# Kernel optimization log

Measured on AMD Instinct MI355X. Metric: run time of the kernel, lower is better.

The kernel has to match this reference:

```python
import jax, jax.numpy as jnp
import numpy as np

B, S, H, D = 4, 1024, 16, 64
DM = H * D  # 1024
SCALE = float(np.sqrt(D))


def setup_inputs() -> dict:
    key = jax.random.key(0)
    ks = jax.random.split(key, 7)
    mk = lambda k, shp: jax.random.normal(k, shp, dtype=jnp.float32)
    return {
        "query": mk(ks[0], (B, S, DM)),
        "key": mk(ks[1], (B, S, DM)),
        "value": mk(ks[2], (B, S, DM)),
        "Wq": mk(ks[3], (DM, DM)) * 0.02,
        "Wk": mk(ks[4], (DM, DM)) * 0.02,
        "Wv": mk(ks[5], (DM, DM)) * 0.02,
        "Wo": mk(ks[6], (DM, DM)) * 0.02,
    }


def reference(query, key, value, Wq, Wk, Wv, Wo):
    b, s, _ = query.shape
    # nn.Linear(x) = x @ W.T ; reshape to (b, h, s, d)
    Q = (query @ Wq.T).reshape(b, s, H, D).transpose(0, 2, 1, 3)
    K = (key @ Wk.T).reshape(b, s, H, D).transpose(0, 2, 1, 3)
    V = (value @ Wv.T).reshape(b, s, H, D).transpose(0, 2, 1, 3)
    scores = jnp.einsum("bhqd,bhkd->bhqk", Q, K) / SCALE
    attn = jax.nn.softmax(scores, axis=-1)  # dropout p=0 -> identity
    ctx = jnp.einsum("bhqk,bhkd->bhqd", attn, V)
    ctx = ctx.transpose(0, 2, 1, 3).reshape(b, s, DM)
    out = ctx @ Wo.T
    return out, attn
```

## Files before the change

### kernel.cpp

```cpp
#include <hip/hip_runtime.h>
#include <hip/hip_bf16.h>
#include <stdint.h>


#define DEV static __device__ __forceinline__

typedef __bf16 bf16x8 __attribute__((ext_vector_type(8)));
typedef float f32x4 __attribute__((ext_vector_type(4)));
typedef unsigned short u16x8 __attribute__((ext_vector_type(8)));

static constexpr int B = 4, S = 1024, H = 16, D = 64, DM = 1024, M = 4096;
static constexpr size_t NQ = (size_t)M * DM;

DEV uint16_t f2bf_bits(float f) {
    __hip_bfloat16 h = __float2bfloat16(f);
    return __builtin_bit_cast(uint16_t, h);
}
DEV uint64_t pack4(float4 v) {
    return (uint64_t)f2bf_bits(v.x) | ((uint64_t)f2bf_bits(v.y) << 16) |
           ((uint64_t)f2bf_bits(v.z) << 32) | ((uint64_t)f2bf_bits(v.w) << 48);
}
DEV uint64_t pack4f(const f32x4& v) {
    return (uint64_t)f2bf_bits(v[0]) | ((uint64_t)f2bf_bits(v[1]) << 16) |
           ((uint64_t)f2bf_bits(v[2]) << 32) | ((uint64_t)f2bf_bits(v[3]) << 48);
}
DEV bf16x8 ldfrag(const uint16_t* p) {
    u16x8 t = *(const u16x8*)p;
    return __builtin_bit_cast(bf16x8, t);
}

#define GLOAD16(g, l)                                                  \
    __builtin_amdgcn_global_load_lds(                                  \
        (const __attribute__((address_space(1))) void*)(g),            \
        (__attribute__((address_space(3))) void*)(l), 16, 0, 0)

#define MFMA16(a, b, c) __builtin_amdgcn_mfma_f32_16x16x32_bf16(a, b, c, 0, 0, 0)

__global__ __launch_bounds__(256) void cvt_all(const float* __restrict__ q,
                                               const float* __restrict__ k,
                                               const float* __restrict__ v,
                                               const float* __restrict__ wq,
                                               const float* __restrict__ wk,
                                               const float* __restrict__ wv,
                                               const float* __restrict__ wo,
                                               uint16_t* __restrict__ dst) {
    const int y = blockIdx.y;
    const float* srcs[7] = {q, k, v, wq, wk, wv, wo};
    const float* src = srcs[y];
    const size_t base = y < 3 ? (size_t)y * NQ : 3 * NQ + (size_t)(y - 3) * (DM * DM);
    const size_t n = y < 3 ? NQ : (size_t)DM * DM;
    size_t i = ((size_t)blockIdx.x * 256 + threadIdx.x) * 8;
    if (i >= n) return;
    float4 a = *(const float4*)(src + i);
    float4 b2 = *(const float4*)(src + i + 4);
    *(uint64_t*)(dst + base + i) = pack4(a);
    *(uint64_t*)(dst + base + i + 4) = pack4(b2);
}

__global__ __launch_bounds__(256) void cvt_w4(const float* __restrict__ w0,
                                              const float* __restrict__ w1,
                                              const float* __restrict__ w2,
                                              const float* __restrict__ w3,
                                              uint16_t* __restrict__ dst) {
    const float* srcs[4] = {w0, w1, w2, w3};
    const float* src = srcs[blockIdx.y];
    uint16_t* d = dst + (size_t)blockIdx.y * DM * DM;
    int i = (blockIdx.x * 256 + threadIdx.x) * 8;
    float4 a = *(const float4*)(src + i);
    float4 b2 = *(const float4*)(src + i + 4);
    *(uint64_t*)(d + i) = pack4(a);
    *(uint64_t*)(d + i + 4) = pack4(b2);
}

template <int AF32>
__global__ __launch_bounds__(256) void gemm_qkv(const float* __restrict__ qa,
                                                const float* __restrict__ ka,
                                                const float* __restrict__ va,
                                                const uint16_t* __restrict__ xb,
                                                const uint16_t* __restrict__ Wb,
                                                uint16_t* __restrict__ Qb,
                                                uint16_t* __restrict__ Kb,
                                                uint16_t* __restrict__ Vt) {
    constexpr int BK = 64, ALD = AF32 ? 72 : 64;
    __shared__ __align__(16) uint16_t smem[17408];
    uint16_t* Ah = smem;
    uint16_t* Bh = smem + (AF32 ? 9216 : 8192);
    const int tid = threadIdx.x, lane = tid & 63, wid = tid >> 6;
    const int lr = lane & 15, lg = lane >> 4;
    const int m0 = blockIdx.x * 128, n0 = blockIdx.y * 128, z = blockIdx.z;
    const int wr = (wid >> 1) * 64, wc = (wid & 1) * 64;

    const float* Af = z == 0 ? qa : (z == 1 ? ka : va);
    const uint16_t* Ab = xb + (size_t)z * NQ;
    const uint16_t* W = Wb + (size_t)z * (DM * DM);

    f32x4 acc[4][4] = {};

    for (int kb = 0; kb < DM / BK; ++kb) {
        if constexpr (AF32) {
#pragma unroll
            for (int i = 0; i < 8; ++i) {
                int f = tid + i * 256;
                int row = f >> 4, c4 = (f & 15) * 4;
                float4 vv = *(const float4*)(Af + (size_t)(m0 + row) * DM + kb * BK + c4);
                *(uint64_t*)&Ah[row * ALD + c4] = pack4(vv);
            }
        } else {
#pragma unroll
            for (int p = 0; p < 4; ++p) {
                int row = p * 32 + (tid >> 3), ce = (tid & 7) * 8;
                GLOAD16(Ab + (size_t)(m0 + row) * DM + kb * BK + ce, Ah + row * 64 + ce);
            }
        }
#pragma unroll
        for (int p = 0; p < 4; ++p) {
            int row = p * 32 + (tid >> 3), ce = (tid & 7) * 8;
            GLOAD16(W + (size_t)(n0 + row) * DM + kb * BK + ce, Bh + row * 64 + ce);
        }
        __syncthreads();

        bf16x8 af[4][2], bw[4][2];
#pragma unroll
        for (int i = 0; i < 4; ++i)
#pragma unroll
            for (int ks = 0; ks < 2; ++ks) {
                af[i][ks] = ldfrag(&Ah[(wr + i * 16 + lr) * ALD + ks * 32 + lg * 8]);
                bw[i][ks] = ldfrag(&Bh[(wc + i * 16 + lr) * 64 + ks * 32 + lg * 8]);
            }
#pragma unroll
        for (int ks = 0; ks < 2; ++ks)
#pragma unroll
            for (int mi = 0; mi < 4; ++mi)
#pragma unroll
                for (int ni = 0; ni < 4; ++ni)
                    acc[mi][ni] = MFMA16(af[mi][ks], bw[ni][ks], acc[mi][ni]);
        __syncthreads();
    }

    if (z != 2) {
        uint16_t* Cp = z == 0 ? Qb : Kb;
#pragma unroll
        for (int mi = 0; mi < 4; ++mi)
#pragma unroll
            for (int ni = 0; ni < 4; ++ni)
#pragma unroll
                for (int r = 0; r < 4; ++r) {
                    int gm = m0 + wr + mi * 16 + lg * 4 + r;
                    int gn = n0 + wc + ni * 16 + lr;
                    int b = gm >> 10, s = gm & 1023, h = gn >> 6, d = gn & 63;
                    Cp[((size_t)(b * H + h) * S + s) * D + d] = f2bf_bits(acc[mi][ni][r]);
                }
    } else {
        uint16_t* T = smem;
#pragma unroll
        for (int mi = 0; mi < 4; ++mi)
#pragma unroll
            for (int ni = 0; ni < 4; ++ni) {
                int row = wc + ni * 16 + lr;
                int colb = wr + mi * 16 + lg * 4;
                *(uint64_t*)&T[row * 136 + colb] = pack4f(acc[mi][ni]);
            }
        __syncthreads();
        const int b = m0 >> 10, s0b = m0 & 1023;
#pragma unroll
        for (int p = 0; p < 8; ++p) {
            int row = p * 16 + (tid >> 4), sl = tid & 15;
            int h = (n0 + row) >> 6, d = (n0 + row) & 63;
            u16x8 val = *(u16x8*)&T[row * 136 + sl * 8];
            *(u16x8*)&Vt[((size_t)(b * H + h) * D + d) * S + s0b + sl * 8] = val;
        }
    }
}

__global__ __launch_bounds__(256) void gemm_o(const uint16_t* __restrict__ ctx,
                                              const uint16_t* __restrict__ Wo,
                                              float* __restrict__ out) {
    constexpr int BK = 64;
    __shared__ __align__(16) uint16_t smem[16384];
    uint16_t* Ah = smem;
    uint16_t* Bh = smem + 8192;
    const int tid = threadIdx.x, lane = tid & 63, wid = tid >> 6;
    const int lr = lane & 15, lg = lane >> 4;
    const int m0 = blockIdx.x * 128, n0 = blockIdx.y * 128;
    const int wr = (wid >> 1) * 64, wc = (wid & 1) * 64;

    f32x4 acc[4][4] = {};

    for (int kb = 0; kb < DM / BK; ++kb) {
#pragma unroll
        for (int p = 0; p < 4; ++p) {
            int row = p * 32 + (tid >> 3), ce = (tid & 7) * 8;
            GLOAD16(ctx + (size_t)(m0 + row) * DM + kb * BK + ce, Ah + row * 64 + ce);
            GLOAD16(Wo + (size_t)(n0 + row) * DM + kb * BK + ce, Bh + row * 64 + ce);
        }
        __syncthreads();

        bf16x8 af[4][2], bw[4][2];
#pragma unroll
        for (int i = 0; i < 4; ++i)
#pragma unroll
            for (int ks = 0; ks < 2; ++ks) {
                af[i][ks] = ldfrag(&Ah[(wr + i * 16 + lr) * 64 + ks * 32 + lg * 8]);
                bw[i][ks] = ldfrag(&Bh[(wc + i * 16 + lr) * 64 + ks * 32 + lg * 8]);
            }
#pragma unroll
        for (int ks = 0; ks < 2; ++ks)
#pragma unroll
            for (int mi = 0; mi < 4; ++mi)
#pragma unroll
                for (int ni = 0; ni < 4; ++ni)
                    acc[mi][ni] = MFMA16(af[mi][ks], bw[ni][ks], acc[mi][ni]);
        __syncthreads();
    }

#pragma unroll
    for (int mi = 0; mi < 4; ++mi)
#pragma unroll
        for (int ni = 0; ni < 4; ++ni)
#pragma unroll
            for (int r = 0; r < 4; ++r) {
                int gm = m0 + wr + mi * 16 + lg * 4 + r;
                int gn = n0 + wc + ni * 16 + lr;
                out[(size_t)gm * DM + gn] = acc[mi][ni][r];
            }
}

__global__ __launch_bounds__(256) void attn_fused(const uint16_t* __restrict__ Qb,
                                                  const uint16_t* __restrict__ Kb,
                                                  const uint16_t* __restrict__ Vt,
                                                  float* __restrict__ attn,
                                                  uint16_t* __restrict__ ctx) {
    __shared__ __align__(16) uint16_t Kl[2][2048];
    __shared__ __align__(16) uint16_t Vl[2][2048];
    __shared__ __align__(16) float pf[4][16 * 36];
    const int tid = threadIdx.x, lane = tid & 63, wid = tid >> 6;
    const int lr = lane & 15, lg = lane >> 4;
    const int wg = blockIdx.x;
    const int xcd = wg & 7, rr_ = wg >> 3;
    const int qt = rr_ & 15, bh = xcd + 8 * (rr_ >> 4);
    const int q0 = qt * 64 + wid * 16;

    const uint16_t* Qp = Qb + ((size_t)bh * S + q0) * D;
    const bf16x8 aq0 = ldfrag(Qp + lr * D + lg * 8);
    const bf16x8 aq1 = ldfrag(Qp + lr * D + 32 + lg * 8);

    const uint16_t* Kbase = Kb + (size_t)bh * S * D;
    const uint16_t* Vbase = Vt + (size_t)bh * D * S;
    constexpr float CEXP = 0.125f * 1.44269504088896340736f;

    const int krow = tid >> 3, kslot = (tid & 7) ^ ((tid >> 3) & 7);
    const int vrow = tid >> 2, vslot = (tid & 3) ^ ((tid >> 3) & 3);

#define STAGE_K(buf, kc) GLOAD16(Kbase + (size_t)((kc)*32 + krow) * D + kslot * 8, &Kl[buf][tid * 8])
#define STAGE_V(buf, kc) GLOAD16(Vbase + (size_t)vrow * S + (kc)*32 + vslot * 8, &Vl[buf][tid * 8])
#define KFRAG(buf, t, h) ldfrag(&Kl[buf][((t)*16 + lr) * 64 + ((((h)*4 + lg) ^ (lr & 7)) * 8)])
#define VFRAG(buf, dt) ldfrag(&Vl[buf][((dt)*16 + lr) * 32 + ((lg ^ ((lr >> 1) & 3)) * 8)])

    float lsum[4] = {0.f, 0.f, 0.f, 0.f};
    STAGE_K(0, 0);
    __syncthreads();
    for (int kc = 0; kc < S / 32; ++kc) {
        const int buf = kc & 1;
        if (kc < S / 32 - 1) STAGE_K(buf ^ 1, kc + 1);
        bf16x8 k00 = KFRAG(buf, 0, 0), k01 = KFRAG(buf, 0, 1);
        bf16x8 k10 = KFRAG(buf, 1, 0), k11 = KFRAG(buf, 1, 1);
        f32x4 s0 = {}, s1 = {};
        s0 = MFMA16(aq0, k00, s0);
        s0 = MFMA16(aq1, k01, s0);
        s1 = MFMA16(aq0, k10, s1);
        s1 = MFMA16(aq1, k11, s1);
#pragma unroll
        for (int r = 0; r < 4; ++r)
            lsum[r] += exp2f(s0[r] * CEXP) + exp2f(s1[r] * CEXP);
        __syncthreads();
    }
#pragma unroll
    for (int r = 0; r < 4; ++r) {
        float v = lsum[r];
        v += __shfl_xor(v, 1);
        v += __shfl_xor(v, 2);
        v += __shfl_xor(v, 4);
        v += __shfl_xor(v, 8);
        lsum[r] = 1.0f / v;
    }

    f32x4 cacc[4] = {};
    float* attn_base = attn + (size_t)bh * S * S + (size_t)q0 * S;
    float* pfw = pf[wid];

    STAGE_K(0, 0);
    STAGE_V(0, 0);
    __syncthreads();
    for (int kc = 0; kc < S / 32; ++kc) {
        const int buf = kc & 1;
        if (kc < S / 32 - 1) {
            STAGE_K(buf ^ 1, kc + 1);
            STAGE_V(buf ^ 1, kc + 1);
        }
        bf16x8 k00 = KFRAG(buf, 0, 0), k01 = KFRAG(buf, 0, 1);
        bf16x8 k10 = KFRAG(buf, 1, 0), k11 = KFRAG(buf, 1, 1);
        f32x4 s0 = {}, s1 = {};
        s0 = MFMA16(aq0, k00, s0);
        s0 = MFMA16(aq1, k01, s0);
        s1 = MFMA16(aq0, k10, s1);
        s1 = MFMA16(aq1, k11, s1);
#pragma unroll
        for (int r = 0; r < 4; ++r) {
            pfw[(lg * 4 + r) * 36 + lr] = exp2f(s0[r] * CEXP) * lsum[r];
            pfw[(lg * 4 + r) * 36 + 16 + lr] = exp2f(s1[r] * CEXP) * lsum[r];
        }
        asm volatile("s_waitcnt lgkmcnt(0)" ::: "memory");
        {
            const float* rp = &pfw[(lane >> 2) * 36 + (lane & 3) * 4];
            float4 a0 = *(const float4*)rp;
            float4 a1 = *(const float4*)(rp + 16);
            float* gp = attn_base + (size_t)(lane >> 2) * S + kc * 32 + (lane & 3) * 4;
            *(float4*)gp = a0;
            *(float4*)(gp + 16) = a1;
        }
        bf16x8 pa;
        {
            const f32x4 p0 = *(const f32x4*)&pfw[lr * 36 + lg * 8];
            const f32x4 p1 = *(const f32x4*)&pfw[lr * 36 + lg * 8 + 4];
            u16x8 pu;
#pragma unroll
            for (int j = 0; j < 4; ++j) {
                pu[j] = f2bf_bits(p0[j]);
                pu[4 + j] = f2bf_bits(p1[j]);
            }
            pa = __builtin_bit_cast(bf16x8, pu);
        }
#pragma unroll
        for (int dt = 0; dt < 4; ++dt) {
            bf16x8 bv = VFRAG(buf, dt);
            cacc[dt] = MFMA16(pa, bv, cacc[dt]);
        }
        __syncthreads();
    }

    const int b = bh >> 4, h = bh & 15;
#pragma unroll
    for (int dt = 0; dt < 4; ++dt)
#pragma unroll
        for (int r = 0; r < 4; ++r) {
            int q = q0 + lg * 4 + r;
            int d = dt * 16 + lr;
            ctx[((size_t)b * S + q) * DM + h * D + d] = f2bf_bits(cacc[dt][r]);
        }
#undef STAGE_K
#undef STAGE_V
#undef KFRAG
#undef VFRAG
}

extern "C" void kernel_launch(void* const* d_in, const int* in_sizes, int n_in,
                              void* d_out, int out_size, void* d_ws, size_t ws_size,
                              hipStream_t stream) {
    const float* q = (const float*)d_in[0];
    const float* k = (const float*)d_in[1];
    const float* v = (const float*)d_in[2];
    const float* Wq = (const float*)d_in[3];
    const float* Wk = (const float*)d_in[4];
    const float* Wv = (const float*)d_in[5];
    const float* Wo = (const float*)d_in[6];

    float* out = (float*)d_out;
    float* attn = out + (size_t)B * S * DM;

    const bool big = ws_size >= (size_t)7 * NQ * 2 + 256;
    dim3 gg(M / 128, DM / 128, 3);

    if (big) {
        uint16_t* xb = (uint16_t*)d_ws;
        uint16_t* Wb = xb + 3 * NQ;
        uint16_t* Qb = Wb + NQ;
        uint16_t* Kb = Qb + NQ;
        uint16_t* Vt = Kb + NQ;
        uint16_t* ctx = xb;
        cvt_all<<<dim3(2048, 7), 256, 0, stream>>>(q, k, v, Wq, Wk, Wv, Wo, xb);
        gemm_qkv<0><<<gg, 256, 0, stream>>>(q, k, v, xb, Wb, Qb, Kb, Vt);
        attn_fused<<<dim3(1024), 256, 0, stream>>>(Qb, Kb, Vt, attn, ctx);
        gemm_o<<<dim3(M / 128, DM / 128), 256, 0, stream>>>(ctx, Wb + (size_t)3 * DM * DM, out);
    } else {
        uint16_t* Qb = (uint16_t*)d_ws;
        uint16_t* Kb = Qb + NQ;
        uint16_t* Vt = Kb + NQ;
        uint16_t* ctx = Vt + NQ;
        uint16_t* Wb = ctx + NQ;
        cvt_w4<<<dim3(512, 4), 256, 0, stream>>>(Wq, Wk, Wv, Wo, Wb);
        gemm_qkv<1><<<gg, 256, 0, stream>>>(q, k, v, nullptr, Wb, Qb, Kb, Vt);
        attn_fused<<<dim3(1024), 256, 0, stream>>>(Qb, Kb, Vt, attn, ctx);
        gemm_o<<<dim3(M / 128, DM / 128), 256, 0, stream>>>(ctx, Wb + (size_t)3 * DM * DM, out);
    }
}
```

Baseline: 456.9 us.

## Split attention key range across warps, drop LDS staging, halve gemm_o N tile

The attention kernel now gives each block 32 queries and has two warps per query group each cover half the key range. The partial softmax denominators and context accumulators are combined through shared memory. K and V fragments are read straight from global memory instead of through double-buffered LDS with per-iteration barriers, and the attn tensor is written with nontemporal stores. This doubles the grid and raises occupancy, at the cost of uncoalesced global fragment loads and a cross-warp reduction. gemm_o switches to 128x64 tiles so it launches more blocks.

```diff
diff --git a/kernel.cpp b/kernel.cpp
--- a/kernel.cpp
+++ b/kernel.cpp
@@ -176,39 +176,46 @@
                                               const uint16_t* __restrict__ Wo,
                                               float* __restrict__ out) {
     constexpr int BK = 64;
-    __shared__ __align__(16) uint16_t smem[16384];
+    __shared__ __align__(16) uint16_t smem[(128 + 64) * BK];
     uint16_t* Ah = smem;
-    uint16_t* Bh = smem + 8192;
+    uint16_t* Bh = smem + 128 * 64;
     const int tid = threadIdx.x, lane = tid & 63, wid = tid >> 6;
     const int lr = lane & 15, lg = lane >> 4;
-    const int m0 = blockIdx.x * 128, n0 = blockIdx.y * 128;
-    const int wr = (wid >> 1) * 64, wc = (wid & 1) * 64;
-
-    f32x4 acc[4][4] = {};
+    const int m0 = blockIdx.x * 128, n0 = blockIdx.y * 64;
+    const int wr = (wid >> 1) * 64, wc = (wid & 1) * 32;
+
+    f32x4 acc[4][2] = {};
 
     for (int kb = 0; kb < DM / BK; ++kb) {
 #pragma unroll
         for (int p = 0; p < 4; ++p) {
             int row = p * 32 + (tid >> 3), ce = (tid & 7) * 8;
             GLOAD16(ctx + (size_t)(m0 + row) * DM + kb * BK + ce, Ah + row * 64 + ce);
+        }
+#pragma unroll
+        for (int p = 0; p < 2; ++p) {
+            int row = p * 32 + (tid >> 3), ce = (tid & 7) * 8;
             GLOAD16(Wo + (size_t)(n0 + row) * DM + kb * BK + ce, Bh + row * 64 + ce);
         }
         __syncthreads();
 
-        bf16x8 af[4][2], bw[4][2];
+        bf16x8 af[4][2], bw[2][2];
 #pragma unroll
         for (int i = 0; i < 4; ++i)
 #pragma unroll
-            for (int ks = 0; ks < 2; ++ks) {
+            for (int ks = 0; ks < 2; ++ks)
                 af[i][ks] = ldfrag(&Ah[(wr + i * 16 + lr) * 64 + ks * 32 + lg * 8]);
+#pragma unroll
+        for (int i = 0; i < 2; ++i)
+#pragma unroll
+            for (int ks = 0; ks < 2; ++ks)
                 bw[i][ks] = ldfrag(&Bh[(wc + i * 16 + lr) * 64 + ks * 32 + lg * 8]);
-            }
 #pragma unroll
         for (int ks = 0; ks < 2; ++ks)
 #pragma unroll
             for (int mi = 0; mi < 4; ++mi)
 #pragma unroll
-                for (int ni = 0; ni < 4; ++ni)
+                for (int ni = 0; ni < 2; ++ni)
                     acc[mi][ni] = MFMA16(af[mi][ks], bw[ni][ks], acc[mi][ni]);
         __syncthreads();
     }
@@ -216,7 +223,7 @@
 #pragma unroll
     for (int mi = 0; mi < 4; ++mi)
 #pragma unroll
-        for (int ni = 0; ni < 4; ++ni)
+        for (int ni = 0; ni < 2; ++ni)
 #pragma unroll
             for (int r = 0; r < 4; ++r) {
                 int gm = m0 + wr + mi * 16 + lg * 4 + r;
@@ -225,45 +232,38 @@
             }
 }
 
-__global__ __launch_bounds__(256) void attn_fused(const uint16_t* __restrict__ Qb,
-                                                  const uint16_t* __restrict__ Kb,
-                                                  const uint16_t* __restrict__ Vt,
-                                                  float* __restrict__ attn,
-                                                  uint16_t* __restrict__ ctx) {
-    __shared__ __align__(16) uint16_t Kl[2][2048];
-    __shared__ __align__(16) uint16_t Vl[2][2048];
+__global__ __launch_bounds__(256, 8) void attn_fused(const uint16_t* __restrict__ Qb,
+                                                     const uint16_t* __restrict__ Kb,
+                                                     const uint16_t* __restrict__ Vt,
+                                                     float* __restrict__ attn,
+                                                     uint16_t* __restrict__ ctx) {
     __shared__ __align__(16) float pf[4][16 * 36];
+    __shared__ __align__(16) float redc[2][16 * 68];
+    __shared__ float redl[2][2][16];
     const int tid = threadIdx.x, lane = tid & 63, wid = tid >> 6;
     const int lr = lane & 15, lg = lane >> 4;
+    const int qg = wid >> 1, kh = wid & 1;
     const int wg = blockIdx.x;
-    const int xcd = wg & 7, rr_ = wg >> 3;
-    const int qt = rr_ & 15, bh = xcd + 8 * (rr_ >> 4);
-    const int q0 = qt * 64 + wid * 16;
+    const int xcd = wg & 7, rr = wg >> 3;
+    const int qt = rr & 31, bh = xcd + 8 * (rr >> 5);
+    const int q0 = qt * 32 + qg * 16;
+    const int kb0 = kh * 512;
 
     const uint16_t* Qp = Qb + ((size_t)bh * S + q0) * D;
     const bf16x8 aq0 = ldfrag(Qp + lr * D + lg * 8);
     const bf16x8 aq1 = ldfrag(Qp + lr * D + 32 + lg * 8);
 
-    const uint16_t* Kbase = Kb + (size_t)bh * S * D;
-    const uint16_t* Vbase = Vt + (size_t)bh * D * S;
+    const uint16_t* Kbase = Kb + ((size_t)bh * S + kb0) * D;
+    const uint16_t* Vbase = Vt + (size_t)bh * D * S + kb0;
     constexpr float CEXP = 0.125f * 1.44269504088896340736f;
 
-    const int krow = tid >> 3, kslot = (tid & 7) ^ ((tid >> 3) & 7);
-    const int vrow = tid >> 2, vslot = (tid & 3) ^ ((tid >> 3) & 3);
-
-#define STAGE_K(buf, kc) GLOAD16(Kbase + (size_t)((kc)*32 + krow) * D + kslot * 8, &Kl[buf][tid * 8])
-#define STAGE_V(buf, kc) GLOAD16(Vbase + (size_t)vrow * S + (kc)*32 + vslot * 8, &Vl[buf][tid * 8])
-#define KFRAG(buf, t, h) ldfrag(&Kl[buf][((t)*16 + lr) * 64 + ((((h)*4 + lg) ^ (lr & 7)) * 8)])
-#define VFRAG(buf, dt) ldfrag(&Vl[buf][((dt)*16 + lr) * 32 + ((lg ^ ((lr >> 1) & 3)) * 8)])
-
     float lsum[4] = {0.f, 0.f, 0.f, 0.f};
-    STAGE_K(0, 0);
-    __syncthreads();
-    for (int kc = 0; kc < S / 32; ++kc) {
-        const int buf = kc & 1;
-        if (kc < S / 32 - 1) STAGE_K(buf ^ 1, kc + 1);
-        bf16x8 k00 = KFRAG(buf, 0, 0), k01 = KFRAG(buf, 0, 1);
-        bf16x8 k10 = KFRAG(buf, 1, 0), k11 = KFRAG(buf, 1, 1);
+    for (int kc = 0; kc < 16; ++kc) {
+        const uint16_t* Kp = Kbase + (size_t)kc * 32 * D;
+        bf16x8 k00 = ldfrag(Kp + lr * D + lg * 8);
+        bf16x8 k01 = ldfrag(Kp + lr * D + 32 + lg * 8);
+        bf16x8 k10 = ldfrag(Kp + (16 + lr) * D + lg * 8);
+        bf16x8 k11 = ldfrag(Kp + (16 + lr) * D + 32 + lg * 8);
         f32x4 s0 = {}, s1 = {};
         s0 = MFMA16(aq0, k00, s0);
         s0 = MFMA16(aq1, k01, s0);
@@ -272,7 +272,6 @@
 #pragma unroll
         for (int r = 0; r < 4; ++r)
             lsum[r] += exp2f(s0[r] * CEXP) + exp2f(s1[r] * CEXP);
-        __syncthreads();
     }
 #pragma unroll
     for (int r = 0; r < 4; ++r) {
@@ -281,24 +280,31 @@
         v += __shfl_xor(v, 2);
         v += __shfl_xor(v, 4);
         v += __shfl_xor(v, 8);
-        lsum[r] = 1.0f / v;
-    }
+        lsum[r] = v;
+    }
+    if (lr == 0) {
+#pragma unroll
+        for (int r = 0; r < 4; ++r) redl[qg][kh][lg * 4 + r] = lsum[r];
+    }
+    __syncthreads();
+    float linv[4];
+#pragma unroll
+    for (int r = 0; r < 4; ++r) linv[r] = 1.0f / (lsum[r] + redl[qg][kh ^ 1][lg * 4 + r]);
 
     f32x4 cacc[4] = {};
-    float* attn_base = attn + (size_t)bh * S * S + (size_t)q0 * S;
+    float* attn_base = attn + (size_t)bh * S * S + (size_t)q0 * S + kb0;
     float* pfw = pf[wid];
 
-    STAGE_K(0, 0);
-    STAGE_V(0, 0);
-    __syncthreads();
-    for (int kc = 0; kc < S / 32; ++kc) {
-        const int buf = kc & 1;
-        if (kc < S / 32 - 1) {
-            STAGE_K(buf ^ 1, kc + 1);
-            STAGE_V(buf ^ 1, kc + 1);
-        }
-        bf16x8 k00 = KFRAG(buf, 0, 0), k01 = KFRAG(buf, 0, 1);
-        bf16x8 k10 = KFRAG(buf, 1, 0), k11 = KFRAG(buf, 1, 1);
+    for (int kc = 0; kc < 16; ++kc) {
+        const uint16_t* Kp = Kbase + (size_t)kc * 32 * D;
+        bf16x8 k00 = ldfrag(Kp + lr * D + lg * 8);
+        bf16x8 k01 = ldfrag(Kp + lr * D + 32 + lg * 8);
+        bf16x8 k10 = ldfrag(Kp + (16 + lr) * D + lg * 8);
+        bf16x8 k11 = ldfrag(Kp + (16 + lr) * D + 32 + lg * 8);
+        bf16x8 bv[4];
+#pragma unroll
+        for (int dt = 0; dt < 4; ++dt)
+            bv[dt] = ldfrag(Vbase + (size_t)(dt * 16 + lr) * S + kc * 32 + lg * 8);
         f32x4 s0 = {}, s1 = {};
         s0 = MFMA16(aq0, k00, s0);
         s0 = MFMA16(aq1, k01, s0);
@@ -306,17 +312,17 @@
         s1 = MFMA16(aq1, k11, s1);
 #pragma unroll
         for (int r = 0; r < 4; ++r) {
-            pfw[(lg * 4 + r) * 36 + lr] = exp2f(s0[r] * CEXP) * lsum[r];
-            pfw[(lg * 4 + r) * 36 + 16 + lr] = exp2f(s1[r] * CEXP) * lsum[r];
+            pfw[(lg * 4 + r) * 36 + lr] = exp2f(s0[r] * CEXP) * linv[r];
+            pfw[(lg * 4 + r) * 36 + 16 + lr] = exp2f(s1[r] * CEXP) * linv[r];
         }
         asm volatile("s_waitcnt lgkmcnt(0)" ::: "memory");
         {
             const float* rp = &pfw[(lane >> 2) * 36 + (lane & 3) * 4];
-            float4 a0 = *(const float4*)rp;
-            float4 a1 = *(const float4*)(rp + 16);
+            f32x4 a0 = *(const f32x4*)rp;
+            f32x4 a1 = *(const f32x4*)(rp + 16);
             float* gp = attn_base + (size_t)(lane >> 2) * S + kc * 32 + (lane & 3) * 4;
-            *(float4*)gp = a0;
-            *(float4*)(gp + 16) = a1;
+            __builtin_nontemporal_store(a0, (f32x4*)gp);
+            __builtin_nontemporal_store(a1, (f32x4*)(gp + 16));
         }
         bf16x8 pa;
         {
@@ -331,26 +337,30 @@
             pa = __builtin_bit_cast(bf16x8, pu);
         }
 #pragma unroll
-        for (int dt = 0; dt < 4; ++dt) {
-            bf16x8 bv = VFRAG(buf, dt);
-            cacc[dt] = MFMA16(pa, bv, cacc[dt]);
-        }
-        __syncthreads();
-    }
-
-    const int b = bh >> 4, h = bh & 15;
-#pragma unroll
-    for (int dt = 0; dt < 4; ++dt)
-#pragma unroll
-        for (int r = 0; r < 4; ++r) {
-            int q = q0 + lg * 4 + r;
-            int d = dt * 16 + lr;
-            ctx[((size_t)b * S + q) * DM + h * D + d] = f2bf_bits(cacc[dt][r]);
-        }
-#undef STAGE_K
-#undef STAGE_V
-#undef KFRAG
-#undef VFRAG
+        for (int dt = 0; dt < 4; ++dt)
+            cacc[dt] = MFMA16(pa, bv[dt], cacc[dt]);
+    }
+
+    if (kh == 1) {
+#pragma unroll
+        for (int dt = 0; dt < 4; ++dt)
+#pragma unroll
+            for (int r = 0; r < 4; ++r)
+                redc[qg][(lg * 4 + r) * 68 + dt * 16 + lr] = cacc[dt][r];
+    }
+    __syncthreads();
+    if (kh == 0) {
+        const int b = bh >> 4, h = bh & 15;
+#pragma unroll
+        for (int dt = 0; dt < 4; ++dt)
+#pragma unroll
+            for (int r = 0; r < 4; ++r) {
+                float v = cacc[dt][r] + redc[qg][(lg * 4 + r) * 68 + dt * 16 + lr];
+                int q = q0 + lg * 4 + r;
+                int d = dt * 16 + lr;
+                ctx[((size_t)b * S + q) * DM + h * D + d] = f2bf_bits(v);
+            }
+    }
 }
 
 extern "C" void kernel_launch(void* const* d_in, const int* in_sizes, int n_in,
@@ -379,8 +389,8 @@
         uint16_t* ctx = xb;
         cvt_all<<<dim3(2048, 7), 256, 0, stream>>>(q, k, v, Wq, Wk, Wv, Wo, xb);
         gemm_qkv<0><<<gg, 256, 0, stream>>>(q, k, v, xb, Wb, Qb, Kb, Vt);
-        attn_fused<<<dim3(1024), 256, 0, stream>>>(Qb, Kb, Vt, attn, ctx);
-        gemm_o<<<dim3(M / 128, DM / 128), 256, 0, stream>>>(ctx, Wb + (size_t)3 * DM * DM, out);
+        attn_fused<<<dim3(2048), 256, 0, stream>>>(Qb, Kb, Vt, attn, ctx);
+        gemm_o<<<dim3(M / 128, DM / 64), 256, 0, stream>>>(ctx, Wb + (size_t)3 * DM * DM, out);
     } else {
         uint16_t* Qb = (uint16_t*)d_ws;
         uint16_t* Kb = Qb + NQ;
@@ -389,7 +399,7 @@
         uint16_t* Wb = ctx + NQ;
         cvt_w4<<<dim3(512, 4), 256, 0, stream>>>(Wq, Wk, Wv, Wo, Wb);
         gemm_qkv<1><<<gg, 256, 0, stream>>>(q, k, v, nullptr, Wb, Qb, Kb, Vt);
-        attn_fused<<<dim3(1024), 256, 0, stream>>>(Qb, Kb, Vt, attn, ctx);
-        gemm_o<<<dim3(M / 128, DM / 128), 256, 0, stream>>>(ctx, Wb + (size_t)3 * DM * DM, out);
-    }
-}
+        attn_fused<<<dim3(2048), 256, 0, stream>>>(Qb, Kb, Vt, attn, ctx);
+        gemm_o<<<dim3(M / 128, DM / 64), 256, 0, stream>>>(ctx, Wb + (size_t)3 * DM * DM, out);
+    }
+}
```

Result: slower. 571.0 us (+25.0%).
